# Optimization experiments

Hardware: AMD Instinct MI355X
Metric: run time of the kernel (lower is better)

## Reference

```python
import jax, jax.numpy as jnp
import numpy as np

N_NODES = 10000


def _gcn_norm(edge_index, edge_weight, n):
    # PyG GCNConv default: add self-loops (weight 1), symmetric normalization.
    ar = jnp.arange(n, dtype=edge_index.dtype)
    ei = jnp.concatenate([edge_index, jnp.stack([ar, ar])], axis=1)
    ew = jnp.concatenate([edge_weight, jnp.ones((n,), edge_weight.dtype)], axis=0)
    row, col = ei[0], ei[1]
    deg = jax.ops.segment_sum(ew, col, num_segments=n)
    dis = jnp.where(deg > 0, jax.lax.rsqrt(jnp.where(deg > 0, deg, 1.0)), 0.0)
    norm = dis[row] * ew * dis[col]
    return row, col, norm


def _gcn_conv(h, W, b, row, col, norm, n):
    hw = h @ W                                    # [N, out]
    msg = norm[:, None] * hw[row]                 # gather + edge scale
    return jax.ops.segment_sum(msg, col, num_segments=n) + b


def setup_inputs() -> dict:
    key = jax.random.key(0)
    ks = jax.random.split(key, 8)
    N, E, D, H1, H2 = N_NODES, 160000, 256, 128, 64
    return {
        "x": jax.random.normal(ks[0], (N, D), jnp.float32),
        "edge_index": jax.random.randint(ks[1], (2, E), 0, N, jnp.int64 if jax.config.jax_enable_x64 else jnp.int32),
        "edge_weight": jax.random.uniform(ks[2], (E,), jnp.float32),
        "noise": jax.random.normal(ks[3], (N, H2), jnp.float32),
        "W1": jax.random.normal(ks[4], (D, H1), jnp.float32) * (1.0 / np.sqrt(D)),
        "b1": jnp.zeros((H1,), jnp.float32),
        "W2": jax.random.normal(ks[5], (H1, H2), jnp.float32) * (1.0 / np.sqrt(H1)),
        "b2": jnp.zeros((H2,), jnp.float32),
        "W3": jax.random.normal(ks[6], (H1, H2), jnp.float32) * (1.0 / np.sqrt(H1)),
        "b3": jnp.zeros((H2,), jnp.float32),
    }


def reference(x, edge_index, edge_weight, noise, W1, b1, W2, b2, W3, b3):
    n = x.shape[0]
    row, col, norm = _gcn_norm(edge_index, edge_weight, n)
    h = jax.nn.relu(_gcn_conv(x, W1, b1, row, col, norm, n))
    mean = _gcn_conv(h, W2, b2, row, col, norm, n)
    log_std = _gcn_conv(h, W3, b3, row, col, norm, n)
    z = mean + noise * jnp.exp(log_std)           # reparameterization
    adj_rec = jax.nn.sigmoid(z @ z.T)             # [N, N] dot-product decode
    return adj_rec
```

## Files before the change

kernel.cpp:

```cpp
#include <hip/hip_runtime.h>


#define Nn 10000
#define Np 10112
#define NpK (Np * 64)

typedef short short8 __attribute__((ext_vector_type(8)));
typedef float f32x4 __attribute__((ext_vector_type(4)));

static __device__ __forceinline__ float sigmoidf(float v) {
  return 1.0f / (1.0f + __expf(-v));
}
static __device__ __forceinline__ unsigned short f32_to_bf16(float f) {
  unsigned int u = __float_as_uint(f);
  unsigned int r = (u + 0x7FFF + ((u >> 16) & 1)) >> 16;
  return (unsigned short)r;
}
static __device__ __forceinline__ float bf16_to_f32(unsigned short s) {
  return __uint_as_float(((unsigned int)s) << 16);
}

__global__ void k_init(float* __restrict__ deg, int* __restrict__ cnt, int n) {
  int i = blockIdx.x * 256 + threadIdx.x;
  if (i < n) { deg[i] = 1.0f; cnt[i] = 0; }
}

__global__ void k_edge_pre(const int* __restrict__ col, const float* __restrict__ ew,
                           float* __restrict__ deg, int* __restrict__ cnt, int E) {
  int e = blockIdx.x * 256 + threadIdx.x;
  if (e < E) { int c = col[e]; atomicAdd(&deg[c], ew[e]); atomicAdd(&cnt[c], 1); }
}

__global__ void k_dis(float* __restrict__ deg, int n) {
  int i = blockIdx.x * 256 + threadIdx.x;
  if (i < n) { float d = deg[i]; deg[i] = (d > 0.0f) ? rsqrtf(d) : 0.0f; }
}

__global__ __launch_bounds__(256) void k_scan(const int* __restrict__ cnt,
                                              int* __restrict__ ofs, int* __restrict__ ofs2,
                                              int n) {
  __shared__ int partial[256];
  const int t = threadIdx.x;
  const int CH = (n + 255) / 256;
  const int start = t * CH;
  int local = 0;
  for (int j = 0; j < CH; ++j) {
    int idx = start + j;
    if (idx < n) local += cnt[idx];
  }
  partial[t] = local;
  __syncthreads();
  for (int off = 1; off < 256; off <<= 1) {
    int x = (t >= off) ? partial[t - off] : 0;
    __syncthreads();
    partial[t] += x;
    __syncthreads();
  }
  int run = partial[t] - local;
  for (int j = 0; j < CH; ++j) {
    int idx = start + j;
    if (idx < n) {
      ofs[idx] = run; ofs2[idx] = run;
      run += cnt[idx];
    }
  }
  if (t == 255) { ofs[n] = run; ofs2[n] = run; }
}

__global__ void k_fill(const int* __restrict__ row, const int* __restrict__ col,
                       const float* __restrict__ ew, const float* __restrict__ dis,
                       int* __restrict__ ofs2, int* __restrict__ csr_src,
                       float* __restrict__ csr_w, int E) {
  int e = blockIdx.x * 256 + threadIdx.x;
  if (e < E) {
    int r = row[e], c = col[e];
    int p = atomicAdd(&ofs2[c], 1);
    csr_src[p] = r;
    csr_w[p] = dis[r] * ew[e] * dis[c];
  }
}

__global__ __launch_bounds__(256) void k_gemm1(const float* __restrict__ x,
                                               const float* __restrict__ W1,
                                               float* __restrict__ hw1) {
  __shared__ float xs[16][68];
  __shared__ float ws[64][128];
  const int tid = threadIdx.x;
  const int row0 = blockIdx.x * 16;
  const int j0 = (tid & 31) * 4;
  const int r0 = (tid >> 5) * 2;
  const int lr = tid >> 4, lk = tid & 15;
  float acc0[4] = {0, 0, 0, 0}, acc1[4] = {0, 0, 0, 0};
  for (int k0 = 0; k0 < 256; k0 += 64) {
    *(float4*)&xs[lr][lk * 4] = *(const float4*)&x[(row0 + lr) * 256 + k0 + lk * 4];
#pragma unroll
    for (int it = 0; it < 8; ++it) {
      int idx4 = tid + it * 256;
      int kk = idx4 >> 5, jq = idx4 & 31;
      *(float4*)&ws[kk][jq * 4] = *(const float4*)&W1[(k0 + kk) * 128 + jq * 4];
    }
    __syncthreads();
#pragma unroll 8
    for (int kk = 0; kk < 64; ++kk) {
      float a0 = xs[r0][kk], a1 = xs[r0 + 1][kk];
      float4 w = *(const float4*)&ws[kk][j0];
      acc0[0] += a0 * w.x; acc0[1] += a0 * w.y; acc0[2] += a0 * w.z; acc0[3] += a0 * w.w;
      acc1[0] += a1 * w.x; acc1[1] += a1 * w.y; acc1[2] += a1 * w.z; acc1[3] += a1 * w.w;
    }
    __syncthreads();
  }
  *(float4*)&hw1[(row0 + r0) * 128 + j0] = make_float4(acc0[0], acc0[1], acc0[2], acc0[3]);
  *(float4*)&hw1[(row0 + r0 + 1) * 128 + j0] = make_float4(acc1[0], acc1[1], acc1[2], acc1[3]);
}

__global__ __launch_bounds__(256) void k_agg(const int* __restrict__ ofs,
                                             const int* __restrict__ csr_src,
                                             const float* __restrict__ csr_w,
                                             const float* __restrict__ feat,
                                             const float* __restrict__ dis,
                                             const float* __restrict__ b,
                                             float* __restrict__ out, int n, int relu_in) {
  int node = blockIdx.x * 4 + (threadIdx.x >> 6);
  if (node >= n) return;
  int f2 = threadIdx.x & 63;
  const float2* featv = (const float2*)feat;
  int s = ofs[node], e = ofs[node + 1];
  float d = dis[node];
  float2 self = featv[node * 64 + f2];
  float2 acc;
  if (relu_in) {
    acc.x = d * d * fmaxf(self.x, 0.0f);
    acc.y = d * d * fmaxf(self.y, 0.0f);
  } else {
    float2 bb = ((const float2*)b)[f2];
    acc.x = d * d * self.x + bb.x;
    acc.y = d * d * self.y + bb.y;
  }
  for (int j = s; j < e; ++j) {
    int r = csr_src[j];
    float wt = csr_w[j];
    float2 v = featv[r * 64 + f2];
    if (relu_in) { v.x = fmaxf(v.x, 0.0f); v.y = fmaxf(v.y, 0.0f); }
    acc.x += wt * v.x;
    acc.y += wt * v.y;
  }
  ((float2*)out)[node * 64 + f2] = acc;
}

__global__ __launch_bounds__(256) void k_gemm2(const float* __restrict__ hagg,
                                               const float* __restrict__ W2, const float* __restrict__ W3,
                                               const float* __restrict__ b2, const float* __restrict__ b3,
                                               float* __restrict__ mean, float* __restrict__ lstd) {
  __shared__ float xs[16][68];
  __shared__ float ws[64][128];
  const int tid = threadIdx.x;
  const int row0 = blockIdx.x * 16;
  const int j0 = (tid & 31) * 4;
  const int r0 = (tid >> 5) * 2;
  const int lr = tid >> 4, lk = tid & 15;
  float acc0[4] = {0, 0, 0, 0}, acc1[4] = {0, 0, 0, 0};
  for (int k0 = 0; k0 < 128; k0 += 64) {
    *(float4*)&xs[lr][lk * 4] = *(const float4*)&hagg[(row0 + lr) * 128 + k0 + lk * 4];
#pragma unroll
    for (int it = 0; it < 8; ++it) {
      int idx4 = tid + it * 256;
      int kk = idx4 >> 5, jq = idx4 & 31;
      int j = jq * 4;
      float4 wv;
      if (j < 64) wv = *(const float4*)&W2[(k0 + kk) * 64 + j];
      else        wv = *(const float4*)&W3[(k0 + kk) * 64 + (j - 64)];
      *(float4*)&ws[kk][j] = wv;
    }
    __syncthreads();
#pragma unroll 8
    for (int kk = 0; kk < 64; ++kk) {
      float a0 = xs[r0][kk], a1 = xs[r0 + 1][kk];
      float4 w = *(const float4*)&ws[kk][j0];
      acc0[0] += a0 * w.x; acc0[1] += a0 * w.y; acc0[2] += a0 * w.z; acc0[3] += a0 * w.w;
      acc1[0] += a1 * w.x; acc1[1] += a1 * w.y; acc1[2] += a1 * w.z; acc1[3] += a1 * w.w;
    }
    __syncthreads();
  }
  if (j0 < 64) {
    float4 bb = *(const float4*)&b2[j0];
    *(float4*)&mean[(row0 + r0) * 64 + j0] =
        make_float4(acc0[0] + bb.x, acc0[1] + bb.y, acc0[2] + bb.z, acc0[3] + bb.w);
    *(float4*)&mean[(row0 + r0 + 1) * 64 + j0] =
        make_float4(acc1[0] + bb.x, acc1[1] + bb.y, acc1[2] + bb.z, acc1[3] + bb.w);
  } else {
    int j = j0 - 64;
    float4 bb = *(const float4*)&b3[j];
    *(float4*)&lstd[(row0 + r0) * 64 + j] =
        make_float4(acc0[0] + bb.x, acc0[1] + bb.y, acc0[2] + bb.z, acc0[3] + bb.w);
    *(float4*)&lstd[(row0 + r0 + 1) * 64 + j] =
        make_float4(acc1[0] + bb.x, acc1[1] + bb.y, acc1[2] + bb.z, acc1[3] + bb.w);
  }
}

__global__ void k_zsplit(const float* __restrict__ mean, const float* __restrict__ lstd,
                         const float* __restrict__ noise,
                         unsigned short* __restrict__ zh, unsigned short* __restrict__ zl) {
  int idx = blockIdx.x * 256 + threadIdx.x;
  if (idx < NpK) {
    float v = 0.0f;
    if (idx < Nn * 64) v = mean[idx] + noise[idx] * __expf(lstd[idx]);
    unsigned short h = f32_to_bf16(v);
    float lo = v - bf16_to_f32(h);
    zh[idx] = h;
    zl[idx] = f32_to_bf16(lo);
  }
}

__global__ __launch_bounds__(256) void k_decode(const unsigned short* __restrict__ zh,
                                                const unsigned short* __restrict__ zl,
                                                float* __restrict__ out, int n) {
  const int tid = threadIdx.x;
  const int wave = tid >> 6, lane = tid & 63;
  const int rows0 = blockIdx.y * 128 + (wave >> 1) * 64;
  const int cols0 = blockIdx.x * 128 + (wave & 1) * 64;
  const int lrow = lane & 15;
  const int quad = lane >> 4;
  f32x4 acc[4][4];
#pragma unroll
  for (int m = 0; m < 4; ++m)
#pragma unroll
    for (int nn = 0; nn < 4; ++nn) acc[m][nn] = (f32x4){0.0f, 0.0f, 0.0f, 0.0f};

#pragma unroll
  for (int s = 0; s < 3; ++s) {
    const unsigned short* A = (s == 2) ? zl : zh;
    const unsigned short* B = (s == 1) ? zl : zh;
#pragma unroll
    for (int kc = 0; kc < 64; kc += 32) {
      const int ko = kc + quad * 8;
      short8 af[4], bf[4];
#pragma unroll
      for (int m = 0; m < 4; ++m)
        af[m] = *(const short8*)&A[(rows0 + m * 16 + lrow) * 64 + ko];
#pragma unroll
      for (int nn = 0; nn < 4; ++nn)
        bf[nn] = *(const short8*)&B[(cols0 + nn * 16 + lrow) * 64 + ko];
#pragma unroll
      for (int m = 0; m < 4; ++m)
#pragma unroll
        for (int nn = 0; nn < 4; ++nn)
          acc[m][nn] = __builtin_amdgcn_mfma_f32_16x16x32_bf16(af[m], bf[nn], acc[m][nn], 0, 0, 0);
    }
  }

  const int crow0 = quad * 4;
#pragma unroll
  for (int m = 0; m < 4; ++m) {
#pragma unroll
    for (int nn = 0; nn < 4; ++nn) {
      int gc = cols0 + nn * 16 + lrow;
      if (gc >= n) continue;
#pragma unroll
      for (int r = 0; r < 4; ++r) {
        int gr = rows0 + m * 16 + crow0 + r;
        if (gr < n) out[(size_t)gr * n + gc] = sigmoidf(acc[m][nn][r]);
      }
    }
  }
}

extern "C" void kernel_launch(void* const* d_in, const int* in_sizes, int n_in,
                              void* d_out, int out_size, void* d_ws, size_t ws_size,
                              hipStream_t stream) {
  const float* x     = (const float*)d_in[0];
  const int*   ei    = (const int*)d_in[1];
  const float* ew    = (const float*)d_in[2];
  const float* noise = (const float*)d_in[3];
  const float* W1    = (const float*)d_in[4];
  const float* b1    = (const float*)d_in[5];
  const float* W2    = (const float*)d_in[6];
  const float* b2    = (const float*)d_in[7];
  const float* W3    = (const float*)d_in[8];
  const float* b3    = (const float*)d_in[9];
  const int E = in_sizes[2];
  const int n = Nn;
  const int* row = ei;
  const int* col = ei + E;

  float* dis = (float*)d_ws;
  unsigned short* zh = (unsigned short*)((char*)d_ws + 10240 * 4);
  unsigned short* zl = zh + NpK;

  float* S    = (float*)d_out;
  float* hw1  = S;
  float* h    = S + 1310720;
  float* hagg = S + 2621440;
  float* mean = S + 3932160;
  float* lstd = S + 4587520;
  float* csr_w  = S + 5242880;
  int* csr_src  = (int*)(S + 5402880);
  int* ofs      = (int*)(S + 5562880);
  int* ofs2     = (int*)(S + 5572896);
  int* cnt      = (int*)(S + 5582912);

  k_init<<<(n + 255) / 256, 256, 0, stream>>>(dis, cnt, n);
  k_edge_pre<<<(E + 255) / 256, 256, 0, stream>>>(col, ew, dis, cnt, E);
  k_dis<<<(n + 255) / 256, 256, 0, stream>>>(dis, n);
  k_scan<<<1, 256, 0, stream>>>(cnt, ofs, ofs2, n);
  k_fill<<<(E + 255) / 256, 256, 0, stream>>>(row, col, ew, dis, ofs2, csr_src, csr_w, E);

  k_gemm1<<<n / 16, 256, 0, stream>>>(x, W1, hw1);
  k_agg<<<(n + 3) / 4, 256, 0, stream>>>(ofs, csr_src, csr_w, hw1, dis, b1, h, n, 0);
  k_agg<<<(n + 3) / 4, 256, 0, stream>>>(ofs, csr_src, csr_w, h, dis, b1, hagg, n, 1);

  k_gemm2<<<n / 16, 256, 0, stream>>>(hagg, W2, W3, b2, b3, mean, lstd);
  k_zsplit<<<(NpK + 255) / 256, 256, 0, stream>>>(mean, lstd, noise, zh, zl);

  dim3 g((n + 127) / 128, (n + 127) / 128);
  k_decode<<<g, 256, 0, stream>>>(zh, zl, (float*)d_out, n);
}
```

Baseline: 618.9 us.

## Fuse z reparameterization into gemm2 and vectorize decode output stores

Merges the mean/log_std GEMM with the reparameterization and bf16 hi/lo split through shared memory, so the mean and lstd buffers and the separate zsplit kernel go away. Padding rows of zh/zl are now zeroed in the init kernel. The decode kernel loads hi and lo fragments once per k-chunk and swaps the MFMA operand order so each lane holds four consecutive columns. That lets it write the 400MB output with float4 nontemporal stores instead of scattered scalar stores. Sigmoid uses the hardware reciprocal approximation, which may slightly change precision.

```diff
diff --git a/kernel.cpp b/kernel.cpp
--- a/kernel.cpp
+++ b/kernel.cpp
@@ -7,9 +7,10 @@
 
 typedef short short8 __attribute__((ext_vector_type(8)));
 typedef float f32x4 __attribute__((ext_vector_type(4)));
+typedef unsigned short ushort4e __attribute__((ext_vector_type(4)));
 
 static __device__ __forceinline__ float sigmoidf(float v) {
-  return 1.0f / (1.0f + __expf(-v));
+  return __builtin_amdgcn_rcpf(1.0f + __expf(-v));
 }
 static __device__ __forceinline__ unsigned short f32_to_bf16(float f) {
   unsigned int u = __float_as_uint(f);
@@ -20,9 +21,11 @@
   return __uint_as_float(((unsigned int)s) << 16);
 }
 
-__global__ void k_init(float* __restrict__ deg, int* __restrict__ cnt, int n) {
+__global__ void k_init(float* __restrict__ deg, int* __restrict__ cnt, int n,
+                       unsigned short* __restrict__ zh, unsigned short* __restrict__ zl) {
   int i = blockIdx.x * 256 + threadIdx.x;
   if (i < n) { deg[i] = 1.0f; cnt[i] = 0; }
+  if (i < (Np - Nn) * 64) { zh[Nn * 64 + i] = 0; zl[Nn * 64 + i] = 0; }
 }
 
 __global__ void k_edge_pre(const int* __restrict__ col, const float* __restrict__ ew,
@@ -147,12 +150,15 @@
   ((float2*)out)[node * 64 + f2] = acc;
 }
 
-__global__ __launch_bounds__(256) void k_gemm2(const float* __restrict__ hagg,
-                                               const float* __restrict__ W2, const float* __restrict__ W3,
-                                               const float* __restrict__ b2, const float* __restrict__ b3,
-                                               float* __restrict__ mean, float* __restrict__ lstd) {
+__global__ __launch_bounds__(256) void k_gemm2z(const float* __restrict__ hagg,
+                                                const float* __restrict__ W2, const float* __restrict__ W3,
+                                                const float* __restrict__ b2, const float* __restrict__ b3,
+                                                const float* __restrict__ noise,
+                                                unsigned short* __restrict__ zh,
+                                                unsigned short* __restrict__ zl) {
   __shared__ float xs[16][68];
   __shared__ float ws[64][128];
+  __shared__ float zs[16][128];
   const int tid = threadIdx.x;
   const int row0 = blockIdx.x * 16;
   const int j0 = (tid & 31) * 4;
@@ -181,33 +187,31 @@
     }
     __syncthreads();
   }
-  if (j0 < 64) {
-    float4 bb = *(const float4*)&b2[j0];
-    *(float4*)&mean[(row0 + r0) * 64 + j0] =
-        make_float4(acc0[0] + bb.x, acc0[1] + bb.y, acc0[2] + bb.z, acc0[3] + bb.w);
-    *(float4*)&mean[(row0 + r0 + 1) * 64 + j0] =
-        make_float4(acc1[0] + bb.x, acc1[1] + bb.y, acc1[2] + bb.z, acc1[3] + bb.w);
-  } else {
-    int j = j0 - 64;
-    float4 bb = *(const float4*)&b3[j];
-    *(float4*)&lstd[(row0 + r0) * 64 + j] =
-        make_float4(acc0[0] + bb.x, acc0[1] + bb.y, acc0[2] + bb.z, acc0[3] + bb.w);
-    *(float4*)&lstd[(row0 + r0 + 1) * 64 + j] =
-        make_float4(acc1[0] + bb.x, acc1[1] + bb.y, acc1[2] + bb.z, acc1[3] + bb.w);
-  }
-}
-
-__global__ void k_zsplit(const float* __restrict__ mean, const float* __restrict__ lstd,
-                         const float* __restrict__ noise,
-                         unsigned short* __restrict__ zh, unsigned short* __restrict__ zl) {
-  int idx = blockIdx.x * 256 + threadIdx.x;
-  if (idx < NpK) {
-    float v = 0.0f;
-    if (idx < Nn * 64) v = mean[idx] + noise[idx] * __expf(lstd[idx]);
-    unsigned short h = f32_to_bf16(v);
-    float lo = v - bf16_to_f32(h);
-    zh[idx] = h;
-    zl[idx] = f32_to_bf16(lo);
+  {
+    float4 bb = (j0 < 64) ? *(const float4*)&b2[j0] : *(const float4*)&b3[j0 - 64];
+    zs[r0][j0 + 0] = acc0[0] + bb.x; zs[r0][j0 + 1] = acc0[1] + bb.y;
+    zs[r0][j0 + 2] = acc0[2] + bb.z; zs[r0][j0 + 3] = acc0[3] + bb.w;
+    zs[r0 + 1][j0 + 0] = acc1[0] + bb.x; zs[r0 + 1][j0 + 1] = acc1[1] + bb.y;
+    zs[r0 + 1][j0 + 2] = acc1[2] + bb.z; zs[r0 + 1][j0 + 3] = acc1[3] + bb.w;
+  }
+  __syncthreads();
+  {
+    const int r = tid >> 4;
+    const int jj = (tid & 15) * 4;
+    float4 mn = *(const float4*)&zs[r][jj];
+    float4 ls = *(const float4*)&zs[r][64 + jj];
+    float4 nz = *(const float4*)&noise[(row0 + r) * 64 + jj];
+    float z0 = mn.x + nz.x * __expf(ls.x);
+    float z1 = mn.y + nz.y * __expf(ls.y);
+    float z2 = mn.z + nz.z * __expf(ls.z);
+    float z3 = mn.w + nz.w * __expf(ls.w);
+    ushort4e h, l;
+    h[0] = f32_to_bf16(z0); l[0] = f32_to_bf16(z0 - bf16_to_f32(h[0]));
+    h[1] = f32_to_bf16(z1); l[1] = f32_to_bf16(z1 - bf16_to_f32(h[1]));
+    h[2] = f32_to_bf16(z2); l[2] = f32_to_bf16(z2 - bf16_to_f32(h[2]));
+    h[3] = f32_to_bf16(z3); l[3] = f32_to_bf16(z3 - bf16_to_f32(h[3]));
+    *(ushort4e*)&zh[(row0 + r) * 64 + jj] = h;
+    *(ushort4e*)&zl[(row0 + r) * 64 + jj] = l;
   }
 }
 
@@ -227,39 +231,43 @@
     for (int nn = 0; nn < 4; ++nn) acc[m][nn] = (f32x4){0.0f, 0.0f, 0.0f, 0.0f};
 
 #pragma unroll
-  for (int s = 0; s < 3; ++s) {
-    const unsigned short* A = (s == 2) ? zl : zh;
-    const unsigned short* B = (s == 1) ? zl : zh;
-#pragma unroll
-    for (int kc = 0; kc < 64; kc += 32) {
-      const int ko = kc + quad * 8;
-      short8 af[4], bf[4];
-#pragma unroll
-      for (int m = 0; m < 4; ++m)
-        af[m] = *(const short8*)&A[(rows0 + m * 16 + lrow) * 64 + ko];
-#pragma unroll
-      for (int nn = 0; nn < 4; ++nn)
-        bf[nn] = *(const short8*)&B[(cols0 + nn * 16 + lrow) * 64 + ko];
-#pragma unroll
-      for (int m = 0; m < 4; ++m)
-#pragma unroll
-        for (int nn = 0; nn < 4; ++nn)
-          acc[m][nn] = __builtin_amdgcn_mfma_f32_16x16x32_bf16(af[m], bf[nn], acc[m][nn], 0, 0, 0);
-    }
-  }
-
-  const int crow0 = quad * 4;
+  for (int kc = 0; kc < 64; kc += 32) {
+    const int ko = kc + quad * 8;
+    short8 rh[4], rl[4], ch[4], cl[4];
+#pragma unroll
+    for (int m = 0; m < 4; ++m) {
+      rh[m] = *(const short8*)&zh[(rows0 + m * 16 + lrow) * 64 + ko];
+      rl[m] = *(const short8*)&zl[(rows0 + m * 16 + lrow) * 64 + ko];
+    }
+#pragma unroll
+    for (int nn = 0; nn < 4; ++nn) {
+      ch[nn] = *(const short8*)&zh[(cols0 + nn * 16 + lrow) * 64 + ko];
+      cl[nn] = *(const short8*)&zl[(cols0 + nn * 16 + lrow) * 64 + ko];
+    }
+#pragma unroll
+    for (int m = 0; m < 4; ++m)
+#pragma unroll
+      for (int nn = 0; nn < 4; ++nn) {
+        acc[m][nn] = __builtin_amdgcn_mfma_f32_16x16x32_bf16(ch[nn], rh[m], acc[m][nn], 0, 0, 0);
+        acc[m][nn] = __builtin_amdgcn_mfma_f32_16x16x32_bf16(cl[nn], rh[m], acc[m][nn], 0, 0, 0);
+        acc[m][nn] = __builtin_amdgcn_mfma_f32_16x16x32_bf16(ch[nn], rl[m], acc[m][nn], 0, 0, 0);
+      }
+  }
+
 #pragma unroll
   for (int m = 0; m < 4; ++m) {
+    int gr = rows0 + m * 16 + lrow;
+    if (gr >= n) continue;
 #pragma unroll
     for (int nn = 0; nn < 4; ++nn) {
-      int gc = cols0 + nn * 16 + lrow;
-      if (gc >= n) continue;
-#pragma unroll
-      for (int r = 0; r < 4; ++r) {
-        int gr = rows0 + m * 16 + crow0 + r;
-        if (gr < n) out[(size_t)gr * n + gc] = sigmoidf(acc[m][nn][r]);
-      }
+      int c0 = cols0 + nn * 16 + quad * 4;
+      if (c0 >= n) continue;
+      f32x4 v;
+      v[0] = sigmoidf(acc[m][nn][0]);
+      v[1] = sigmoidf(acc[m][nn][1]);
+      v[2] = sigmoidf(acc[m][nn][2]);
+      v[3] = sigmoidf(acc[m][nn][3]);
+      __builtin_nontemporal_store(v, (f32x4*)&out[(size_t)gr * n + c0]);
     }
   }
 }
@@ -290,15 +298,13 @@
   float* hw1  = S;
   float* h    = S + 1310720;
   float* hagg = S + 2621440;
-  float* mean = S + 3932160;
-  float* lstd = S + 4587520;
   float* csr_w  = S + 5242880;
   int* csr_src  = (int*)(S + 5402880);
   int* ofs      = (int*)(S + 5562880);
   int* ofs2     = (int*)(S + 5572896);
   int* cnt      = (int*)(S + 5582912);
 
-  k_init<<<(n + 255) / 256, 256, 0, stream>>>(dis, cnt, n);
+  k_init<<<(n + 255) / 256, 256, 0, stream>>>(dis, cnt, n, zh, zl);
   k_edge_pre<<<(E + 255) / 256, 256, 0, stream>>>(col, ew, dis, cnt, E);
   k_dis<<<(n + 255) / 256, 256, 0, stream>>>(dis, n);
   k_scan<<<1, 256, 0, stream>>>(cnt, ofs, ofs2, n);
@@ -308,8 +314,7 @@
   k_agg<<<(n + 3) / 4, 256, 0, stream>>>(ofs, csr_src, csr_w, hw1, dis, b1, h, n, 0);
   k_agg<<<(n + 3) / 4, 256, 0, stream>>>(ofs, csr_src, csr_w, h, dis, b1, hagg, n, 1);
 
-  k_gemm2<<<n / 16, 256, 0, stream>>>(hagg, W2, W3, b2, b3, mean, lstd);
-  k_zsplit<<<(NpK + 255) / 256, 256, 0, stream>>>(mean, lstd, noise, zh, zl);
+  k_gemm2z<<<n / 16, 256, 0, stream>>>(hagg, W2, W3, b2, b3, noise, zh, zl);
 
   dim3 g((n + 127) / 128, (n + 127) / 128);
   k_decode<<<g, 256, 0, stream>>>(zh, zl, (float*)d_out, n);
```

Measured after the change: 605.5 us. -2.2%, faster.
